# Kernel tuning notes

Hardware: AMD Instinct MI355X
Metric: run time of the kernel (lower is better)

The kernel has to match this reference:

```python
import jax, jax.numpy as jnp
import numpy as np
import math

N_HEADS = 8
EMB = 128
KEY_DIM = EMB // N_HEADS  # 16
B, NQ, T = 32, 1024, 1024


def _uniform(key, shape, stdv):
    return jax.random.uniform(key, shape, jnp.float32, -stdv, stdv)


def setup_inputs() -> dict:
    key = jax.random.key(0)
    ks = jax.random.split(key, 7)
    stdv = 1.0 / math.sqrt(KEY_DIM)      # last dim of w_query/w_key/w_value
    stdv_o = 1.0 / math.sqrt(EMB)        # last dim of w_out
    q = jax.random.normal(ks[0], (B, NQ, EMB), jnp.float32)
    h = jax.random.normal(ks[1], (B, T, EMB), jnp.float32)
    mask = jax.random.randint(ks[2], (B, NQ, T), 0, 2).astype(bool)
    return {
        "q": q,
        "h": h,
        "mask": mask,
        "w_query": _uniform(ks[3], (N_HEADS, EMB, KEY_DIM), stdv),
        "w_key": _uniform(ks[4], (N_HEADS, EMB, KEY_DIM), stdv),
        "w_value": _uniform(ks[5], (N_HEADS, EMB, KEY_DIM), stdv),
        "w_out": _uniform(ks[6], (N_HEADS, KEY_DIM, EMB), stdv_o),
    }


def reference(q, h, mask, w_query, w_key, w_value, w_out):
    # q: [B, NQ, E], h: [B, T, E], mask: [B, NQ, T] (True = blocked)
    scale = 1.0 / math.sqrt(KEY_DIM)
    Q = jnp.einsum('bqi,hik->hbqk', q, w_query)   # [H,B,NQ,dk]
    K = jnp.einsum('bti,hik->hbtk', h, w_key)     # [H,B,T,dk]
    V = jnp.einsum('bti,hiv->hbtv', h, w_value)   # [H,B,T,dv]
    U = scale * jnp.einsum('hbqk,hbtk->hbqt', Q, K)  # [H,B,NQ,T]
    m = mask[None]                                   # broadcast over heads
    U = jnp.where(m, -jnp.inf, U)
    attn = jax.nn.softmax(U, axis=-1)
    attn = jnp.where(m, 0.0, attn)                   # explicit zeroing as in original
    heads = jnp.einsum('hbqt,hbtv->hbqv', attn, V)   # [H,B,NQ,dv]
    out = jnp.einsum('hbqv,hve->bqe', heads, w_out)  # [B,NQ,E]
    return out
```

## Files before the change

kernel.cpp:

```cpp
#include <hip/hip_runtime.h>
#include <hip/hip_bf16.h>
#include <stdint.h>


typedef __attribute__((ext_vector_type(8))) short bf16x8;
typedef __attribute__((ext_vector_type(4))) float f32x4;
typedef __attribute__((ext_vector_type(16))) float f32x16;

#define NEGBIG (-1e30f)
#define QSCALE 0.36067376022224085f
#define EXP2(x) __builtin_amdgcn_exp2f(x)
#define PSTRIDE 68

__device__ __forceinline__ unsigned short f2bf(float x) {
  union { __hip_bfloat16 h; unsigned short u; } cv;
  cv.h = __float2bfloat16(x);
  return cv.u;
}
__device__ __forceinline__ unsigned int pk2bf(float a, float b) {
  unsigned int ua = __float_as_uint(a) + 0x8000u;
  unsigned int ub = __float_as_uint(b) + 0x8000u;
  return __builtin_amdgcn_perm(ub, ua, 0x07060302u);
}
__device__ __forceinline__ unsigned int pk2bf_t(float a, float b) {
  return __builtin_amdgcn_perm(__float_as_uint(b), __float_as_uint(a), 0x07060302u);
}

__global__ __launch_bounds__(256) void projmask_k(const float* __restrict__ qp,
                                                  const float* __restrict__ hp,
                                                  const float* __restrict__ wqp,
                                                  const float* __restrict__ wkp,
                                                  const float* __restrict__ wvp,
                                                  const void* __restrict__ mask,
                                                  unsigned short* __restrict__ Qb,
                                                  unsigned short* __restrict__ Kb,
                                                  unsigned short* __restrict__ Vt,
                                                  unsigned long long* __restrict__ mp64) {
  __shared__ unsigned short WtLds[128 * 136];
  __shared__ __align__(16) unsigned short Cxf[9216];
  const int tid = threadIdx.x;

  if (blockIdx.x >= 1536) {
    const int bx = blockIdx.x - 1536;
    unsigned short* mlds = WtLds;
    const unsigned int* mi = (const unsigned int*)mask;
    unsigned int accv = 0;
    #pragma unroll
    for (int k = 0; k < 16; ++k) accv |= mi[k * 251];
    const bool bytemode = accv > 1u;

    const long long i0 = ((long long)bx * 256 + tid) * 16;
    unsigned int v = 0;
    if (bytemode) {
      int4 w = *(const int4*)((const unsigned char*)mask + i0);
      unsigned int ws[4] = {(unsigned)w.x, (unsigned)w.y, (unsigned)w.z, (unsigned)w.w};
      #pragma unroll
      for (int d = 0; d < 4; ++d)
        #pragma unroll
        for (int j = 0; j < 4; ++j)
          v |= (((ws[d] >> (8*j)) & 0xFFu) ? 1u : 0u) << (d*4 + j);
    } else {
      const int4* mp4 = (const int4*)((const int*)mask + i0);
      #pragma unroll
      for (int d = 0; d < 4; ++d) {
        int4 w = mp4[d];
        v |= (w.x ? 1u : 0u) << (d*4 + 0);
        v |= (w.y ? 1u : 0u) << (d*4 + 1);
        v |= (w.z ? 1u : 0u) << (d*4 + 2);
        v |= (w.w ? 1u : 0u) << (d*4 + 3);
      }
    }
    mlds[tid] = (unsigned short)v;
    __syncthreads();
    if (tid < 64)
      mp64[(long long)bx * 64 + tid] = ((const unsigned long long*)mlds)[tid];
    return;
  }

  const int wave = tid >> 6, lane = tid & 63;
  const int llo4 = lane & 15, lhi4 = lane >> 4;
  const int xb = blockIdx.x & 511;
  const int sel = blockIdx.x >> 9;
  const int m0 = xb * 64;
  const int b = m0 >> 10, row0 = m0 & 1023;
  const float* A = (sel == 0) ? qp : hp;
  const float* W = (sel == 0) ? wqp : (sel == 1) ? wkp : wvp;
  const float wscale = (sel == 0) ? QSCALE : 1.0f;

  #pragma unroll
  for (int i = 0; i < 8; ++i) {
    int base = (tid + i * 256) * 8;
    float4 w0 = *(const float4*)&W[base];
    float4 w1 = *(const float4*)&W[base + 4];
    float wv8[8] = {w0.x, w0.y, w0.z, w0.w, w1.x, w1.y, w1.z, w1.w};
    #pragma unroll
    for (int j = 0; j < 8; ++j) {
      int idx = base + j;
      int h = idx >> 11, e = (idx >> 4) & 127, kk = idx & 15;
      WtLds[(h*16 + kk) * 136 + e] = f2bf(wv8[j] * wscale);
    }
  }
  #pragma unroll
  for (int i = 0; i < 4; ++i) {
    int r = (tid >> 4) + i * 16;
    int c = (tid & 15) * 8;
    float4 a0 = *(const float4*)&A[(m0 + r) * 128 + c];
    float4 a1 = *(const float4*)&A[(m0 + r) * 128 + c + 4];
    bf16x8 a8;
    a8[0] = (short)f2bf(a0.x); a8[1] = (short)f2bf(a0.y);
    a8[2] = (short)f2bf(a0.z); a8[3] = (short)f2bf(a0.w);
    a8[4] = (short)f2bf(a1.x); a8[5] = (short)f2bf(a1.y);
    a8[6] = (short)f2bf(a1.z); a8[7] = (short)f2bf(a1.w);
    *(bf16x8*)&Cxf[r * 136 + c] = a8;
  }
  __syncthreads();

  const int n0 = wave * 32;
  f32x4 acc[4][2] = {};
  #pragma unroll
  for (int kk = 0; kk < 128; kk += 32) {
    bf16x8 af[4], bfr[2];
    #pragma unroll
    for (int mi2 = 0; mi2 < 4; ++mi2)
      af[mi2] = *(const bf16x8*)&Cxf[(mi2*16 + llo4)*136 + kk + lhi4*8];
    #pragma unroll
    for (int ni = 0; ni < 2; ++ni)
      bfr[ni] = *(const bf16x8*)&WtLds[(n0 + ni*16 + llo4)*136 + kk + lhi4*8];
    #pragma unroll
    for (int mi2 = 0; mi2 < 4; ++mi2)
      #pragma unroll
      for (int ni = 0; ni < 2; ++ni)
        acc[mi2][ni] = __builtin_amdgcn_mfma_f32_16x16x32_bf16(af[mi2], bfr[ni], acc[mi2][ni], 0, 0, 0);
  }

  __syncthreads();
  if (sel < 2) {
    unsigned short* Cb = sel ? Kb : Qb;
    #pragma unroll
    for (int mi2 = 0; mi2 < 4; ++mi2)
      #pragma unroll
      for (int ni = 0; ni < 2; ++ni) {
        int n = n0 + ni*16 + llo4;
        #pragma unroll
        for (int r = 0; r < 4; ++r)
          Cxf[(mi2*16 + lhi4*4 + r)*136 + n] = f2bf(acc[mi2][ni][r]);
      }
    __syncthreads();
    #pragma unroll
    for (int it = 0; it < 4; ++it) {
      int u = tid + it*256;
      int h = u >> 7, rk = u & 127, row = rk >> 1, kh = rk & 1;
      bf16x8 vv = *(const bf16x8*)&Cxf[row*136 + h*16 + kh*8];
      *(bf16x8*)&Cb[((b*8 + h)*1024 + row0 + row)*16 + kh*8] = vv;
    }
  } else {
    #pragma unroll
    for (int mi2 = 0; mi2 < 4; ++mi2)
      #pragma unroll
      for (int ni = 0; ni < 2; ++ni) {
        int n = n0 + ni*16 + llo4;
        ushort4 pk;
        pk.x = f2bf(acc[mi2][ni][0]); pk.y = f2bf(acc[mi2][ni][1]);
        pk.z = f2bf(acc[mi2][ni][2]); pk.w = f2bf(acc[mi2][ni][3]);
        *(ushort4*)&Cxf[n*72 + mi2*16 + lhi4*4] = pk;
      }
    __syncthreads();
    #pragma unroll
    for (int it = 0; it < 4; ++it) {
      int u = tid + it*256;
      int n = u >> 3, tc = u & 7;
      int h = n >> 4, k = n & 15;
      bf16x8 vv = *(const bf16x8*)&Cxf[n*72 + tc*8];
      *(bf16x8*)&Vt[((b*8 + h)*16 + k)*1024 + row0 + tc*8] = vv;
    }
  }
}

__global__ __launch_bounds__(64) void attn_k(const unsigned short* __restrict__ Qb,
                                             const unsigned short* __restrict__ Kb,
                                             const unsigned short* __restrict__ Vtb,
                                             const unsigned long long* __restrict__ mp64,
                                             unsigned short* __restrict__ heads) {
  __shared__ __align__(16) unsigned short Pw[32 * PSTRIDE];
  __shared__ __align__(8) uint2 mlut[16];
  const int lane = threadIdx.x;
  const int llo4 = lane & 15, lhi4 = lane >> 4;
  const int llo5 = lane & 31, lhi5 = lane >> 5;
  const int q0 = blockIdx.x * 32;
  const int b  = blockIdx.y;
  const int h  = blockIdx.z;
  const int bh = b * 8 + h;
  const unsigned long long* mp_base = &mp64[((b << 10) + q0 + llo5) * 16];
  const unsigned short* Kbase = &Kb[(bh * 1024 + llo5) * 16 + lhi5 * 8];
  const unsigned short* Vbase = &Vtb[(bh * 16 + llo4) * 1024 + lhi4 * 8];

  if (lane < 16) {
    unsigned int n = lane;
    unsigned int h0 = (n & 1u) ? 0u : 0xFFFFu;
    unsigned int h1 = (n & 2u) ? 0u : 0xFFFFu;
    unsigned int h2 = (n & 4u) ? 0u : 0xFFFFu;
    unsigned int h3 = (n & 8u) ? 0u : 0xFFFFu;
    mlut[lane] = make_uint2(h0 | (h1 << 16), h2 | (h3 << 16));
  }

  bf16x8 qf = *(const bf16x8*)&Qb[(bh * 1024 + q0 + llo5) * 16 + lhi5 * 8];

  bf16x8 ones;
  #pragma unroll
  for (int j = 0; j < 8; ++j) ones[j] = (short)0x3F80;
  f32x16 cb16;
  #pragma unroll
  for (int j = 0; j < 16; ++j) cb16[j] = -18.f;

  f32x4 ot[2] = {};
  f32x4 lacc[2] = {};

  bf16x8 kfb[2][2], vfb[2][2];
  unsigned long long mwb[2];

  #pragma unroll
  for (int tt = 0; tt < 2; ++tt)
    kfb[0][tt] = *(const bf16x8*)&Kbase[(tt*32) * 16];
  #pragma unroll
  for (int kt = 0; kt < 2; ++kt)
    vfb[0][kt] = *(const bf16x8*)&Vbase[kt*32];
  mwb[0] = mp_base[0];

  #pragma unroll 2
  for (int tw = 0; tw < 16; ++tw) {
    const int cur = tw & 1, nxt = cur ^ 1;
    const int twn = (tw < 15) ? tw + 1 : 15;
    const int t0n = twn * 64;
    #pragma unroll
    for (int tt = 0; tt < 2; ++tt)
      kfb[nxt][tt] = *(const bf16x8*)&Kbase[(t0n + tt*32) * 16];
    #pragma unroll
    for (int kt = 0; kt < 2; ++kt)
      vfb[nxt][kt] = *(const bf16x8*)&Vbase[t0n + kt*32];
    mwb[nxt] = mp_base[twn];

    f32x16 st[2];
    #pragma unroll
    for (int tt = 0; tt < 2; ++tt)
      st[tt] = __builtin_amdgcn_mfma_f32_32x32x16_bf16(kfb[cur][tt], qf, cb16, 0, 0, 0);

    const unsigned int mwlo = (unsigned int)mwb[cur];
    const unsigned int mwhi = (unsigned int)(mwb[cur] >> 32);
    #pragma unroll
    for (int tt = 0; tt < 2; ++tt) {
      const unsigned int m32 = (tt ? mwhi : mwlo) >> (lhi5 * 4);
      #pragma unroll
      for (int g = 0; g < 4; ++g) {
        unsigned int nib = (m32 >> (g*8)) & 0xFu;
        uint2 am = mlut[nib];
        uint2 d;
        d.x = pk2bf_t(EXP2(st[tt][g*4 + 0]), EXP2(st[tt][g*4 + 1])) & am.x;
        d.y = pk2bf_t(EXP2(st[tt][g*4 + 2]), EXP2(st[tt][g*4 + 3])) & am.y;
        *(uint2*)&Pw[llo5 * PSTRIDE + tt*32 + lhi5*4 + g*8] = d;
      }
    }

    #pragma unroll
    for (int kt = 0; kt < 2; ++kt) {
      #pragma unroll
      for (int qn = 0; qn < 2; ++qn) {
        const unsigned short* pp = &Pw[(qn*16 + llo4) * PSTRIDE + kt*32 + lhi4*8];
        uint2 p0 = *(const uint2*)pp;
        uint2 p1 = *(const uint2*)(pp + 4);
        union { uint2 u[2]; bf16x8 v; } pf;
        pf.u[0] = p0; pf.u[1] = p1;
        ot[qn]   = __builtin_amdgcn_mfma_f32_16x16x32_bf16(vfb[cur][kt], pf.v, ot[qn], 0, 0, 0);
        lacc[qn] = __builtin_amdgcn_mfma_f32_16x16x32_bf16(ones,        pf.v, lacc[qn], 0, 0, 0);
      }
    }
  }

  #pragma unroll
  for (int qn = 0; qn < 2; ++qn) {
    float l = lacc[qn][0];
    float inv = l > 0.f ? 1.f / l : 0.f;
    f32x4 o = ot[qn] * inv;
    uint2 d;
    d.x = pk2bf(o[0], o[1]);
    d.y = pk2bf(o[2], o[3]);
    *(uint2*)&heads[((b << 10) + q0 + qn*16 + llo4) * 128 + h*16 + lhi4*4] = d;
  }
}

__global__ __launch_bounds__(256) void outproj_k(const unsigned short* __restrict__ Av,
                                                 const float* __restrict__ W,
                                                 float* __restrict__ Co) {
  __shared__ unsigned short WtLds[128 * 136];
  __shared__ __align__(16) unsigned short Cxf[9216];
  const int tid = threadIdx.x;
  const int wave = tid >> 6, lane = tid & 63;
  const int llo4 = lane & 15, lhi4 = lane >> 4;
  const int m0 = blockIdx.x * 64;

  #pragma unroll
  for (int i = 0; i < 8; ++i) {
    int base = (tid + i * 256) * 8;
    float4 w0 = *(const float4*)&W[base];
    float4 w1 = *(const float4*)&W[base + 4];
    float wv8[8] = {w0.x, w0.y, w0.z, w0.w, w1.x, w1.y, w1.z, w1.w};
    #pragma unroll
    for (int j = 0; j < 8; ++j) {
      int idx = base + j;
      WtLds[(idx & 127) * 136 + (idx >> 7)] = f2bf(wv8[j]);
    }
  }
  #pragma unroll
  for (int i = 0; i < 4; ++i) {
    int r = (tid >> 4) + i * 16;
    int c = (tid & 15) * 8;
    *(bf16x8*)&Cxf[r * 136 + c] = *(const bf16x8*)&Av[(m0 + r) * 128 + c];
  }
  __syncthreads();

  const int n0 = wave * 32;
  f32x4 acc[4][2] = {};
  #pragma unroll
  for (int kk = 0; kk < 128; kk += 32) {
    bf16x8 af[4], bfr[2];
    #pragma unroll
    for (int mi2 = 0; mi2 < 4; ++mi2)
      af[mi2] = *(const bf16x8*)&Cxf[(mi2*16 + llo4)*136 + kk + lhi4*8];
    #pragma unroll
    for (int ni = 0; ni < 2; ++ni)
      bfr[ni] = *(const bf16x8*)&WtLds[(n0 + ni*16 + llo4)*136 + kk + lhi4*8];
    #pragma unroll
    for (int mi2 = 0; mi2 < 4; ++mi2)
      #pragma unroll
      for (int ni = 0; ni < 2; ++ni)
        acc[mi2][ni] = __builtin_amdgcn_mfma_f32_16x16x32_bf16(af[mi2], bfr[ni], acc[mi2][ni], 0, 0, 0);
  }
  #pragma unroll
  for (int mi2 = 0; mi2 < 4; ++mi2)
    #pragma unroll
    for (int ni = 0; ni < 2; ++ni) {
      int n = n0 + ni*16 + llo4;
      int mbase = m0 + mi2*16 + lhi4*4;
      #pragma unroll
      for (int r = 0; r < 4; ++r)
        Co[(mbase + r) * 128 + n] = acc[mi2][ni][r];
    }
}

extern "C" void kernel_launch(void* const* d_in, const int* in_sizes, int n_in,
                              void* d_out, int out_size, void* d_ws, size_t ws_size,
                              hipStream_t stream) {
  const float* q  = (const float*)d_in[0];
  const float* hh = (const float*)d_in[1];
  const void*  mk = d_in[2];
  const float* wq = (const float*)d_in[3];
  const float* wk = (const float*)d_in[4];
  const float* wv = (const float*)d_in[5];
  const float* wo = (const float*)d_in[6];
  float* out = (float*)d_out;

  unsigned short* Qb = (unsigned short*)d_ws;
  unsigned short* Kb = Qb + 32*8*1024*16;
  unsigned short* Vt = Kb + 32*8*1024*16;
  unsigned short* hd = Vt + 32*8*1024*16;
  unsigned long long* mp64 = (unsigned long long*)(hd + 32768*128);

  projmask_k<<<9728, 256, 0, stream>>>(q, hh, wq, wk, wv, mk, Qb, Kb, Vt, mp64);
  attn_k<<<dim3(32, 32, 8), 64, 0, stream>>>(Qb, Kb, Vt, mp64, hd);
  outproj_k<<<512, 256, 0, stream>>>(hd, wo, out);
}
```

Baseline: 302.3 us.

## Process 64 queries per attention block, remap grid for XCD locality, add setprio

Each attention workgroup now handles two 32-query halves, so every K/V fragment load is reused across 64 queries. The grid is flattened to 4096 blocks, with a swizzled block-id mapping meant to keep blocks of the same batch and head on one XCD for L2 reuse. s_setprio is raised around the MFMA sections so matrix work gets issue priority over waves doing exp/mask work. The cost is half as many blocks, more registers per wave, and a serialised reuse of the single Pw buffer across the two query halves.

```diff
diff --git a/kernel.cpp b/kernel.cpp
--- a/kernel.cpp
+++ b/kernel.cpp
@@ -186,9 +186,11 @@
   const int lane = threadIdx.x;
   const int llo4 = lane & 15, lhi4 = lane >> 4;
   const int llo5 = lane & 31, lhi5 = lane >> 5;
-  const int q0 = blockIdx.x * 32;
-  const int b  = blockIdx.y;
-  const int h  = blockIdx.z;
+  const int bid = blockIdx.x;
+  const int nid = (bid & 7) * 512 + (bid >> 3);
+  const int q0 = (nid & 15) * 64;
+  const int b  = (nid >> 4) & 31;
+  const int h  = nid >> 9;
   const int bh = b * 8 + h;
   const unsigned long long* mp_base = &mp64[((b << 10) + q0 + llo5) * 16];
   const unsigned short* Kbase = &Kb[(bh * 1024 + llo5) * 16 + lhi5 * 8];
@@ -203,7 +205,10 @@
     mlut[lane] = make_uint2(h0 | (h1 << 16), h2 | (h3 << 16));
   }
 
-  bf16x8 qf = *(const bf16x8*)&Qb[(bh * 1024 + q0 + llo5) * 16 + lhi5 * 8];
+  bf16x8 qf[2];
+  #pragma unroll
+  for (int qh = 0; qh < 2; ++qh)
+    qf[qh] = *(const bf16x8*)&Qb[(bh * 1024 + q0 + qh*32 + llo5) * 16 + lhi5 * 8];
 
   bf16x8 ones;
   #pragma unroll
@@ -212,11 +217,11 @@
   #pragma unroll
   for (int j = 0; j < 16; ++j) cb16[j] = -18.f;
 
-  f32x4 ot[2] = {};
-  f32x4 lacc[2] = {};
+  f32x4 ot[2][2] = {};
+  f32x4 lacc[2][2] = {};
 
   bf16x8 kfb[2][2], vfb[2][2];
-  unsigned long long mwb[2];
+  unsigned long long mwb[2][2];
 
   #pragma unroll
   for (int tt = 0; tt < 2; ++tt)
@@ -224,7 +229,8 @@
   #pragma unroll
   for (int kt = 0; kt < 2; ++kt)
     vfb[0][kt] = *(const bf16x8*)&Vbase[kt*32];
-  mwb[0] = mp_base[0];
+  mwb[0][0] = mp_base[0];
+  mwb[0][1] = mp_base[512];
 
   #pragma unroll 2
   for (int tw = 0; tw < 16; ++tw) {
@@ -237,54 +243,64 @@
     #pragma unroll
     for (int kt = 0; kt < 2; ++kt)
       vfb[nxt][kt] = *(const bf16x8*)&Vbase[t0n + kt*32];
-    mwb[nxt] = mp_base[twn];
-
-    f32x16 st[2];
-    #pragma unroll
-    for (int tt = 0; tt < 2; ++tt)
-      st[tt] = __builtin_amdgcn_mfma_f32_32x32x16_bf16(kfb[cur][tt], qf, cb16, 0, 0, 0);
-
-    const unsigned int mwlo = (unsigned int)mwb[cur];
-    const unsigned int mwhi = (unsigned int)(mwb[cur] >> 32);
-    #pragma unroll
-    for (int tt = 0; tt < 2; ++tt) {
-      const unsigned int m32 = (tt ? mwhi : mwlo) >> (lhi5 * 4);
-      #pragma unroll
-      for (int g = 0; g < 4; ++g) {
-        unsigned int nib = (m32 >> (g*8)) & 0xFu;
-        uint2 am = mlut[nib];
-        uint2 d;
-        d.x = pk2bf_t(EXP2(st[tt][g*4 + 0]), EXP2(st[tt][g*4 + 1])) & am.x;
-        d.y = pk2bf_t(EXP2(st[tt][g*4 + 2]), EXP2(st[tt][g*4 + 3])) & am.y;
-        *(uint2*)&Pw[llo5 * PSTRIDE + tt*32 + lhi5*4 + g*8] = d;
-      }
-    }
-
-    #pragma unroll
-    for (int kt = 0; kt < 2; ++kt) {
-      #pragma unroll
-      for (int qn = 0; qn < 2; ++qn) {
-        const unsigned short* pp = &Pw[(qn*16 + llo4) * PSTRIDE + kt*32 + lhi4*8];
-        uint2 p0 = *(const uint2*)pp;
-        uint2 p1 = *(const uint2*)(pp + 4);
-        union { uint2 u[2]; bf16x8 v; } pf;
-        pf.u[0] = p0; pf.u[1] = p1;
-        ot[qn]   = __builtin_amdgcn_mfma_f32_16x16x32_bf16(vfb[cur][kt], pf.v, ot[qn], 0, 0, 0);
-        lacc[qn] = __builtin_amdgcn_mfma_f32_16x16x32_bf16(ones,        pf.v, lacc[qn], 0, 0, 0);
-      }
-    }
-  }
-
-  #pragma unroll
-  for (int qn = 0; qn < 2; ++qn) {
-    float l = lacc[qn][0];
-    float inv = l > 0.f ? 1.f / l : 0.f;
-    f32x4 o = ot[qn] * inv;
-    uint2 d;
-    d.x = pk2bf(o[0], o[1]);
-    d.y = pk2bf(o[2], o[3]);
-    *(uint2*)&heads[((b << 10) + q0 + qn*16 + llo4) * 128 + h*16 + lhi4*4] = d;
-  }
+    mwb[nxt][0] = mp_base[twn];
+    mwb[nxt][1] = mp_base[512 + twn];
+
+    #pragma unroll
+    for (int qh = 0; qh < 2; ++qh) {
+      f32x16 st[2];
+      __builtin_amdgcn_s_setprio(1);
+      #pragma unroll
+      for (int tt = 0; tt < 2; ++tt)
+        st[tt] = __builtin_amdgcn_mfma_f32_32x32x16_bf16(kfb[cur][tt], qf[qh], cb16, 0, 0, 0);
+      __builtin_amdgcn_s_setprio(0);
+
+      const unsigned int mwlo = (unsigned int)mwb[cur][qh];
+      const unsigned int mwhi = (unsigned int)(mwb[cur][qh] >> 32);
+      #pragma unroll
+      for (int tt = 0; tt < 2; ++tt) {
+        const unsigned int m32 = (tt ? mwhi : mwlo) >> (lhi5 * 4);
+        #pragma unroll
+        for (int g = 0; g < 4; ++g) {
+          unsigned int nib = (m32 >> (g*8)) & 0xFu;
+          uint2 am = mlut[nib];
+          uint2 d;
+          d.x = pk2bf_t(EXP2(st[tt][g*4 + 0]), EXP2(st[tt][g*4 + 1])) & am.x;
+          d.y = pk2bf_t(EXP2(st[tt][g*4 + 2]), EXP2(st[tt][g*4 + 3])) & am.y;
+          *(uint2*)&Pw[llo5 * PSTRIDE + tt*32 + lhi5*4 + g*8] = d;
+        }
+      }
+
+      __builtin_amdgcn_s_setprio(1);
+      #pragma unroll
+      for (int kt = 0; kt < 2; ++kt) {
+        #pragma unroll
+        for (int qn = 0; qn < 2; ++qn) {
+          const unsigned short* pp = &Pw[(qn*16 + llo4) * PSTRIDE + kt*32 + lhi4*8];
+          uint2 p0 = *(const uint2*)pp;
+          uint2 p1 = *(const uint2*)(pp + 4);
+          union { uint2 u[2]; bf16x8 v; } pf;
+          pf.u[0] = p0; pf.u[1] = p1;
+          ot[qh][qn]   = __builtin_amdgcn_mfma_f32_16x16x32_bf16(vfb[cur][kt], pf.v, ot[qh][qn], 0, 0, 0);
+          lacc[qh][qn] = __builtin_amdgcn_mfma_f32_16x16x32_bf16(ones,         pf.v, lacc[qh][qn], 0, 0, 0);
+        }
+      }
+      __builtin_amdgcn_s_setprio(0);
+    }
+  }
+
+  #pragma unroll
+  for (int qh = 0; qh < 2; ++qh)
+    #pragma unroll
+    for (int qn = 0; qn < 2; ++qn) {
+      float l = lacc[qh][qn][0];
+      float inv = l > 0.f ? 1.f / l : 0.f;
+      f32x4 o = ot[qh][qn] * inv;
+      uint2 d;
+      d.x = pk2bf(o[0], o[1]);
+      d.y = pk2bf(o[2], o[3]);
+      *(uint2*)&heads[((b << 10) + q0 + qh*32 + qn*16 + llo4) * 128 + h*16 + lhi4*4] = d;
+    }
 }
 
 __global__ __launch_bounds__(256) void outproj_k(const unsigned short* __restrict__ Av,
@@ -365,6 +381,6 @@
   unsigned long long* mp64 = (unsigned long long*)(hd + 32768*128);
 
   projmask_k<<<9728, 256, 0, stream>>>(q, hh, wq, wk, wv, mk, Qb, Kb, Vt, mp64);
-  attn_k<<<dim3(32, 32, 8), 64, 0, stream>>>(Qb, Kb, Vt, mp64, hd);
+  attn_k<<<4096, 64, 0, stream>>>(Qb, Kb, Vt, mp64, hd);
   outproj_k<<<512, 256, 0, stream>>>(hd, wo, out);
 }
```

New measurement: 297.8 us. Within noise of the previous version (-1.5%).
